# Performance work log

Measured on AMD Instinct MI355X. Metric: run time of the kernel, lower is better.

## Reference

```python
import jax, jax.numpy as jnp
import numpy as np

ALPHA = 0.2  # LeakyReLU negative slope
NEG_INF = -9e15


def setup_inputs() -> dict:
    key = jax.random.key(0)
    k1, k2, k3, k4, k5 = jax.random.split(key, 5)
    N, F_in, F_out = 8192, 128, 64
    h = jax.random.normal(k1, (N, F_in), dtype=jnp.float32)
    adj = jax.random.randint(k2, (N, N), 0, 2, dtype=jnp.int32)
    edge_feat = jax.random.normal(k3, (N, N), dtype=jnp.float32)
    W = jax.random.normal(k4, (F_in, F_out), dtype=jnp.float32) * 0.1
    a = jax.random.normal(k5, (2 * F_out + 1, 1), dtype=jnp.float32) * 0.1
    return {"h": h, "adj": adj, "edge_feat": edge_feat, "W": W, "a": a}


def reference(h, adj, edge_feat, W, a):
    # Wh: [N, F']
    Wh = h @ W
    F_out = W.shape[1]
    # Decompose the linear score over the concatenated features:
    # e[i,j] = leakyrelu( Wh[i].a1 + Wh[j].a2 + edge_feat[i,j]*a_e )
    a1 = a[:F_out, 0]          # applied to source (row i) features
    a2 = a[F_out:2 * F_out, 0]  # applied to target (col j) features
    a_e = a[2 * F_out, 0]       # applied to scalar edge feature
    s1 = Wh @ a1               # [N]
    s2 = Wh @ a2               # [N]
    e = s1[:, None] + s2[None, :] + edge_feat * a_e  # [N, N]
    e = jnp.where(e > 0, e, ALPHA * e)  # LeakyReLU
    e = jnp.where(adj > 0, e, NEG_INF)
    attention = jax.nn.softmax(e, axis=1)  # [N, N]
    h_prime = attention @ Wh               # [N, F']
    return jax.nn.elu(h_prime)
```

## Files before the change

kernel.cpp:

```cpp
#include <hip/hip_runtime.h>
#include <hip/hip_bf16.h>

#define N_NODES 8192
#define F_IN    128
#define F_OUT   64
#define GAT_ALPHA 0.2f
#define JSPLIT  16
#define COLS_PER_SPLIT (N_NODES / JSPLIT)
#define KC      128
#define NCHUNK  (COLS_PER_SPLIT / KC)
#define LDSTR   136

typedef short  short8_t  __attribute__((ext_vector_type(8)));
typedef float  f32x4_t   __attribute__((ext_vector_type(4)));

static __device__ __forceinline__ unsigned int f32_to_bf16_bits(float x) {
    unsigned int u = __float_as_uint(x);
    return (u + 0x7fffu + ((u >> 16) & 1u)) >> 16;
}

__global__ __launch_bounds__(256) void k_wh(
    const float* __restrict__ h, const float* __restrict__ W, const float* __restrict__ a,
    unsigned short* __restrict__ wht, float* __restrict__ s1, float* __restrict__ s2)
{
    __shared__ float Wl[F_IN][F_OUT];
    int tid = threadIdx.x;
    #pragma unroll
    for (int i = 0; i < (F_IN * F_OUT) / 256; ++i) {
        int idx = tid + i * 256;
        Wl[idx >> 6][idx & 63] = W[idx];
    }
    __syncthreads();
    int wave = tid >> 6, lane = tid & 63;
    int row = blockIdx.x * 4 + wave;
    const float* hr = h + (size_t)row * F_IN;
    float acc = 0.f;
    #pragma unroll
    for (int k = 0; k < F_IN; k += 4) {
        float4 hv = *(const float4*)(hr + k);
        acc += hv.x * Wl[k + 0][lane];
        acc += hv.y * Wl[k + 1][lane];
        acc += hv.z * Wl[k + 2][lane];
        acc += hv.w * Wl[k + 3][lane];
    }
    wht[(size_t)lane * N_NODES + row] = (unsigned short)f32_to_bf16_bits(acc);
    float p1 = acc * a[lane];
    float p2 = acc * a[F_OUT + lane];
    #pragma unroll
    for (int off = 32; off > 0; off >>= 1) {
        p1 += __shfl_down(p1, off);
        p2 += __shfl_down(p2, off);
    }
    if (lane == 0) { s1[row] = p1; s2[row] = p2; }
}

__global__ __launch_bounds__(256, 4) void k_attn(
    const int* __restrict__ adj, const float* __restrict__ ef,
    const float* __restrict__ a,
    const float* __restrict__ s1, const float* __restrict__ s2,
    const unsigned short* __restrict__ wht,
    float* __restrict__ Osum, float* __restrict__ lsum)
{
    __shared__ unsigned short pl[64 * LDSTR];
    int tid  = threadIdx.x;
    int wave = tid >> 6, lane = tid & 63;
    int q = lane >> 4, m = lane & 15;
    int rowtile = blockIdx.x / JSPLIT;
    int split   = blockIdx.x % JSPLIT;
    int row0  = rowtile * 64;
    int jbase = split * COLS_PER_SPLIT;

    int ca  = (tid & 31) * 4;
    int ra0 = tid >> 5;
    float a_e = a[2 * F_OUT];
    float s1v[8];
    #pragma unroll
    for (int i = 0; i < 8; ++i) s1v[i] = s1[row0 + i * 8 + ra0];

    const unsigned short* wm = wht + (size_t)m * N_NODES + jbase;

    f32x4_t acc0 = {0.f, 0.f, 0.f, 0.f};
    f32x4_t acc1 = acc0, acc2 = acc0, acc3 = acc0, accl = acc0;
    short8_t ones;
    #pragma unroll
    for (int i = 0; i < 8; ++i) ones[i] = (short)0x3F80;

    for (int ch = 0; ch < NCHUNK; ++ch) {
        int cb = jbase + ch * KC + ca;
        float4 s2q = *(const float4*)(s2 + cb);
        int4   aj[8];
        float4 ev[8];
        #pragma unroll
        for (int i = 0; i < 8; ++i) {
            size_t off = (size_t)(row0 + i * 8 + ra0) * N_NODES + cb;
            aj[i] = *(const int4*)(adj + off);
            ev[i] = *(const float4*)(ef + off);
        }
        #pragma unroll
        for (int i = 0; i < 8; ++i) {
            float b0 = s1v[i] + s2q.x, b1 = s1v[i] + s2q.y;
            float b2 = s1v[i] + s2q.z, b3 = s1v[i] + s2q.w;
            float e0 = fmaf(ev[i].x, a_e, b0); e0 = fmaxf(e0, GAT_ALPHA * e0);
            float e1 = fmaf(ev[i].y, a_e, b1); e1 = fmaxf(e1, GAT_ALPHA * e1);
            float e2 = fmaf(ev[i].z, a_e, b2); e2 = fmaxf(e2, GAT_ALPHA * e2);
            float e3 = fmaf(ev[i].w, a_e, b3); e3 = fmaxf(e3, GAT_ALPHA * e3);
            float p0 = (aj[i].x > 0) ? __expf(e0) : 0.f;
            float p1 = (aj[i].y > 0) ? __expf(e1) : 0.f;
            float p2 = (aj[i].z > 0) ? __expf(e2) : 0.f;
            float p3 = (aj[i].w > 0) ? __expf(e3) : 0.f;
            uint2 pk;
            pk.x = f32_to_bf16_bits(p0) | (f32_to_bf16_bits(p1) << 16);
            pk.y = f32_to_bf16_bits(p2) | (f32_to_bf16_bits(p3) << 16);
            *(uint2*)&pl[(i * 8 + ra0) * LDSTR + ca] = pk;
        }
        __syncthreads();
        int arow = (wave * 16 + m) * LDSTR;
        #pragma unroll
        for (int kk = 0; kk < 4; ++kk) {
            short8_t af = *(const short8_t*)&pl[arow + kk * 32 + q * 8];
            const unsigned short* wp = wm + ch * KC + kk * 32 + q * 8;
            short8_t b0 = *(const short8_t*)(wp);
            short8_t b1 = *(const short8_t*)(wp + (size_t)16 * N_NODES);
            short8_t b2 = *(const short8_t*)(wp + (size_t)32 * N_NODES);
            short8_t b3 = *(const short8_t*)(wp + (size_t)48 * N_NODES);
            acc0 = __builtin_amdgcn_mfma_f32_16x16x32_bf16(af, b0, acc0, 0, 0, 0);
            acc1 = __builtin_amdgcn_mfma_f32_16x16x32_bf16(af, b1, acc1, 0, 0, 0);
            acc2 = __builtin_amdgcn_mfma_f32_16x16x32_bf16(af, b2, acc2, 0, 0, 0);
            acc3 = __builtin_amdgcn_mfma_f32_16x16x32_bf16(af, b3, acc3, 0, 0, 0);
            accl = __builtin_amdgcn_mfma_f32_16x16x32_bf16(af, ones, accl, 0, 0, 0);
        }
        __syncthreads();
    }

    #pragma unroll
    for (int r = 0; r < 4; ++r) {
        int orow = row0 + wave * 16 + q * 4 + r;
        float* op = Osum + (size_t)orow * F_OUT + m;
        atomicAdd(op +  0, acc0[r]);
        atomicAdd(op + 16, acc1[r]);
        atomicAdd(op + 32, acc2[r]);
        atomicAdd(op + 48, acc3[r]);
    }
    if (m == 0) {
        #pragma unroll
        for (int r = 0; r < 4; ++r)
            atomicAdd(&lsum[row0 + wave * 16 + q * 4 + r], accl[r]);
    }
}

__global__ __launch_bounds__(256) void k_out(
    const float* __restrict__ Osum, const float* __restrict__ lsum, float* __restrict__ out)
{
    int i = blockIdx.x * 256 + threadIdx.x;
    float v = Osum[i] / lsum[i >> 6];
    out[i] = (v > 0.f) ? v : (__expf(v) - 1.f);
}

extern "C" void kernel_launch(void* const* d_in, const int* in_sizes, int n_in,
                              void* d_out, int out_size, void* d_ws, size_t ws_size,
                              hipStream_t stream)
{
    const float* h   = (const float*)d_in[0];
    const int*   adj = (const int*)d_in[1];
    const float* ef  = (const float*)d_in[2];
    const float* W   = (const float*)d_in[3];
    const float* a   = (const float*)d_in[4];
    float* out = (float*)d_out;

    char* ws = (char*)d_ws;
    unsigned short* wht = (unsigned short*)ws;
    float* s1   = (float*)(ws + (size_t)F_OUT * N_NODES * 2);
    float* s2   = s1 + N_NODES;
    float* Osum = s2 + N_NODES;
    float* lsum = Osum + (size_t)N_NODES * F_OUT;

    hipMemsetAsync(Osum, 0, ((size_t)N_NODES * F_OUT + N_NODES) * sizeof(float), stream);

    k_wh  <<<N_NODES / 4, 256, 0, stream>>>(h, W, a, wht, s1, s2);
    k_attn<<<(N_NODES / 64) * JSPLIT, 256, 0, stream>>>(adj, ef, a, s1, s2, wht, Osum, lsum);
    k_out <<<(N_NODES * F_OUT) / 256, 256, 0, stream>>>(Osum, lsum, out);
}
```

Baseline: 557.6 us.

## Give each wave private LDS tiles and prefetch next chunk without block barriers

Each wave now computes its own 16 rows of attention probabilities into a private double-buffered LDS region, so the block-wide __syncthreads are removed. The adjacency, edge-feature and s2 loads for the next 64-column chunk are issued before the current chunk's LDS write and MFMAs, and the Wh^T operands are loaded early in registers. The aim is to hide global-memory latency and barrier stalls in this bandwidth-bound kernel. In exchange the chunk size halves, register pressure rises, and the occupancy hint in launch_bounds is dropped. Each lane reads a 16-column strip of one row, which changes the coalescing pattern.

```diff
diff --git a/kernel.cpp b/kernel.cpp
--- a/kernel.cpp
+++ b/kernel.cpp
@@ -7,9 +7,9 @@
 #define GAT_ALPHA 0.2f
 #define JSPLIT  16
 #define COLS_PER_SPLIT (N_NODES / JSPLIT)
-#define KC      128
-#define NCHUNK  (COLS_PER_SPLIT / KC)
-#define LDSTR   136
+#define KC      64
+#define NCH     (COLS_PER_SPLIT / KC)
+#define LSTR    72
 
 typedef short  short8_t  __attribute__((ext_vector_type(8)));
 typedef float  f32x4_t   __attribute__((ext_vector_type(4)));
@@ -54,29 +54,31 @@
     if (lane == 0) { s1[row] = p1; s2[row] = p2; }
 }
 
-__global__ __launch_bounds__(256, 4) void k_attn(
+__global__ __launch_bounds__(256) void k_attn(
     const int* __restrict__ adj, const float* __restrict__ ef,
     const float* __restrict__ a,
     const float* __restrict__ s1, const float* __restrict__ s2,
     const unsigned short* __restrict__ wht,
     float* __restrict__ Osum, float* __restrict__ lsum)
 {
-    __shared__ unsigned short pl[64 * LDSTR];
+    __shared__ unsigned short pl[4 * 2 * 16 * LSTR];
     int tid  = threadIdx.x;
     int wave = tid >> 6, lane = tid & 63;
     int q = lane >> 4, m = lane & 15;
+    int r  = lane >> 2;
+    int cq = lane & 3;
     int rowtile = blockIdx.x / JSPLIT;
     int split   = blockIdx.x % JSPLIT;
-    int row0  = rowtile * 64;
+    int row0  = rowtile * 64 + wave * 16;
     int jbase = split * COLS_PER_SPLIT;
 
-    int ca  = (tid & 31) * 4;
-    int ra0 = tid >> 5;
     float a_e = a[2 * F_OUT];
-    float s1v[8];
-    #pragma unroll
-    for (int i = 0; i < 8; ++i) s1v[i] = s1[row0 + i * 8 + ra0];
-
+    int Rr = row0 + r;
+    float s1v = s1[Rr];
+    const int*   adjr = adj + (size_t)Rr * N_NODES + jbase + cq * 16;
+    const float* efr  = ef  + (size_t)Rr * N_NODES + jbase + cq * 16;
+    const float* s2r  = s2 + jbase + cq * 16;
+    unsigned short* plw = pl + wave * (2 * 16 * LSTR);
     const unsigned short* wm = wht + (size_t)m * N_NODES + jbase;
 
     f32x4_t acc0 = {0.f, 0.f, 0.f, 0.f};
@@ -85,66 +87,80 @@
     #pragma unroll
     for (int i = 0; i < 8; ++i) ones[i] = (short)0x3F80;
 
-    for (int ch = 0; ch < NCHUNK; ++ch) {
-        int cb = jbase + ch * KC + ca;
-        float4 s2q = *(const float4*)(s2 + cb);
-        int4   aj[8];
-        float4 ev[8];
+    int4   aj[4];
+    float4 ev[4], sv[4];
+    #pragma unroll
+    for (int u = 0; u < 4; ++u) {
+        aj[u] = *(const int4*)  (adjr + u * 4);
+        ev[u] = *(const float4*)(efr  + u * 4);
+        sv[u] = *(const float4*)(s2r  + u * 4);
+    }
+
+    #pragma unroll 2
+    for (int ch = 0; ch < NCH; ++ch) {
+        const unsigned short* wp = wm + ch * KC + q * 8;
+        short8_t b[8];
         #pragma unroll
-        for (int i = 0; i < 8; ++i) {
-            size_t off = (size_t)(row0 + i * 8 + ra0) * N_NODES + cb;
-            aj[i] = *(const int4*)(adj + off);
-            ev[i] = *(const float4*)(ef + off);
+        for (int kk = 0; kk < 2; ++kk)
+            #pragma unroll
+            for (int t = 0; t < 4; ++t)
+                b[kk * 4 + t] = *(const short8_t*)(wp + (size_t)t * 16 * N_NODES + kk * 32);
+
+        uint2 pk[4];
+        #pragma unroll
+        for (int u = 0; u < 4; ++u) {
+            float e0 = fmaf(ev[u].x, a_e, s1v + sv[u].x); e0 = fmaxf(e0, GAT_ALPHA * e0);
+            float e1 = fmaf(ev[u].y, a_e, s1v + sv[u].y); e1 = fmaxf(e1, GAT_ALPHA * e1);
+            float e2 = fmaf(ev[u].z, a_e, s1v + sv[u].z); e2 = fmaxf(e2, GAT_ALPHA * e2);
+            float e3 = fmaf(ev[u].w, a_e, s1v + sv[u].w); e3 = fmaxf(e3, GAT_ALPHA * e3);
+            float p0 = (aj[u].x > 0) ? __expf(e0) : 0.f;
+            float p1 = (aj[u].y > 0) ? __expf(e1) : 0.f;
+            float p2 = (aj[u].z > 0) ? __expf(e2) : 0.f;
+            float p3 = (aj[u].w > 0) ? __expf(e3) : 0.f;
+            pk[u].x = f32_to_bf16_bits(p0) | (f32_to_bf16_bits(p1) << 16);
+            pk[u].y = f32_to_bf16_bits(p2) | (f32_to_bf16_bits(p3) << 16);
         }
+
+        if (ch + 1 < NCH) {
+            adjr += KC; efr += KC; s2r += KC;
+            #pragma unroll
+            for (int u = 0; u < 4; ++u) {
+                aj[u] = *(const int4*)  (adjr + u * 4);
+                ev[u] = *(const float4*)(efr  + u * 4);
+                sv[u] = *(const float4*)(s2r  + u * 4);
+            }
+        }
+
+        unsigned short* pb = plw + (ch & 1) * (16 * LSTR);
         #pragma unroll
-        for (int i = 0; i < 8; ++i) {
-            float b0 = s1v[i] + s2q.x, b1 = s1v[i] + s2q.y;
-            float b2 = s1v[i] + s2q.z, b3 = s1v[i] + s2q.w;
-            float e0 = fmaf(ev[i].x, a_e, b0); e0 = fmaxf(e0, GAT_ALPHA * e0);
-            float e1 = fmaf(ev[i].y, a_e, b1); e1 = fmaxf(e1, GAT_ALPHA * e1);
-            float e2 = fmaf(ev[i].z, a_e, b2); e2 = fmaxf(e2, GAT_ALPHA * e2);
-            float e3 = fmaf(ev[i].w, a_e, b3); e3 = fmaxf(e3, GAT_ALPHA * e3);
-            float p0 = (aj[i].x > 0) ? __expf(e0) : 0.f;
-            float p1 = (aj[i].y > 0) ? __expf(e1) : 0.f;
-            float p2 = (aj[i].z > 0) ? __expf(e2) : 0.f;
-            float p3 = (aj[i].w > 0) ? __expf(e3) : 0.f;
-            uint2 pk;
-            pk.x = f32_to_bf16_bits(p0) | (f32_to_bf16_bits(p1) << 16);
-            pk.y = f32_to_bf16_bits(p2) | (f32_to_bf16_bits(p3) << 16);
-            *(uint2*)&pl[(i * 8 + ra0) * LDSTR + ca] = pk;
-        }
-        __syncthreads();
-        int arow = (wave * 16 + m) * LDSTR;
+        for (int u = 0; u < 4; ++u)
+            *(uint2*)&pb[r * LSTR + cq * 16 + u * 4] = pk[u];
+
+        const unsigned short* pr = pb + m * LSTR;
         #pragma unroll
-        for (int kk = 0; kk < 4; ++kk) {
-            short8_t af = *(const short8_t*)&pl[arow + kk * 32 + q * 8];
-            const unsigned short* wp = wm + ch * KC + kk * 32 + q * 8;
-            short8_t b0 = *(const short8_t*)(wp);
-            short8_t b1 = *(const short8_t*)(wp + (size_t)16 * N_NODES);
-            short8_t b2 = *(const short8_t*)(wp + (size_t)32 * N_NODES);
-            short8_t b3 = *(const short8_t*)(wp + (size_t)48 * N_NODES);
-            acc0 = __builtin_amdgcn_mfma_f32_16x16x32_bf16(af, b0, acc0, 0, 0, 0);
-            acc1 = __builtin_amdgcn_mfma_f32_16x16x32_bf16(af, b1, acc1, 0, 0, 0);
-            acc2 = __builtin_amdgcn_mfma_f32_16x16x32_bf16(af, b2, acc2, 0, 0, 0);
-            acc3 = __builtin_amdgcn_mfma_f32_16x16x32_bf16(af, b3, acc3, 0, 0, 0);
+        for (int kk = 0; kk < 2; ++kk) {
+            short8_t af = *(const short8_t*)&pr[kk * 32 + q * 8];
+            acc0 = __builtin_amdgcn_mfma_f32_16x16x32_bf16(af, b[kk * 4 + 0], acc0, 0, 0, 0);
+            acc1 = __builtin_amdgcn_mfma_f32_16x16x32_bf16(af, b[kk * 4 + 1], acc1, 0, 0, 0);
+            acc2 = __builtin_amdgcn_mfma_f32_16x16x32_bf16(af, b[kk * 4 + 2], acc2, 0, 0, 0);
+            acc3 = __builtin_amdgcn_mfma_f32_16x16x32_bf16(af, b[kk * 4 + 3], acc3, 0, 0, 0);
             accl = __builtin_amdgcn_mfma_f32_16x16x32_bf16(af, ones, accl, 0, 0, 0);
         }
-        __syncthreads();
     }
 
     #pragma unroll
-    for (int r = 0; r < 4; ++r) {
-        int orow = row0 + wave * 16 + q * 4 + r;
+    for (int rr = 0; rr < 4; ++rr) {
+        int orow = row0 + q * 4 + rr;
         float* op = Osum + (size_t)orow * F_OUT + m;
-        atomicAdd(op +  0, acc0[r]);
-        atomicAdd(op + 16, acc1[r]);
-        atomicAdd(op + 32, acc2[r]);
-        atomicAdd(op + 48, acc3[r]);
+        atomicAdd(op +  0, acc0[rr]);
+        atomicAdd(op + 16, acc1[rr]);
+        atomicAdd(op + 32, acc2[rr]);
+        atomicAdd(op + 48, acc3[rr]);
     }
     if (m == 0) {
         #pragma unroll
-        for (int r = 0; r < 4; ++r)
-            atomicAdd(&lsum[row0 + wave * 16 + q * 4 + r], accl[r]);
+        for (int rr = 0; rr < 4; ++rr)
+            atomicAdd(&lsum[row0 + q * 4 + rr], accl[rr]);
     }
 }
 
```

After: 548.9 us. About the same (-1.6%).
